# Kernel tuning notes

Hardware: AMD Instinct MI355X
Metric: run time of the kernel (lower is better)

The kernel has to match this reference:

```python
import jax, jax.numpy as jnp
import numpy as np

D_MODEL = 1024
N_HEADS = 16
D_HEAD = D_MODEL // N_HEADS
D_FF = 4 * D_MODEL
SEQ = 2048
BATCH = 4
EPS = 1e-5


def setup_inputs() -> dict:
    key = jax.random.key(0)
    ks = jax.random.split(key, 12)
    s = 0.02
    return {
        "x": jax.random.normal(ks[0], (BATCH, SEQ, D_MODEL), dtype=jnp.float32),
        "ln1_g": jnp.ones((D_MODEL,), jnp.float32),
        "ln1_b": jnp.zeros((D_MODEL,), jnp.float32),
        "wq": jax.random.normal(ks[1], (N_HEADS, D_MODEL, D_HEAD), jnp.float32) * s,
        "bq": jnp.zeros((N_HEADS, D_HEAD), jnp.float32),
        "wk": jax.random.normal(ks[2], (N_HEADS, D_MODEL, D_HEAD), jnp.float32) * s,
        "bk": jnp.zeros((N_HEADS, D_HEAD), jnp.float32),
        "wv": jax.random.normal(ks[3], (N_HEADS, D_MODEL, D_HEAD), jnp.float32) * s,
        "bv": jnp.zeros((N_HEADS, D_HEAD), jnp.float32),
        "wp": jax.random.normal(ks[4], (D_MODEL, D_MODEL), jnp.float32) * s,
        "bp": jnp.zeros((D_MODEL,), jnp.float32),
        "ln2_g": jnp.ones((D_MODEL,), jnp.float32),
        "ln2_b": jnp.zeros((D_MODEL,), jnp.float32),
        "w1": jax.random.normal(ks[5], (D_MODEL, D_FF), jnp.float32) * s,
        "b1": jnp.zeros((D_FF,), jnp.float32),
        "w2": jax.random.normal(ks[6], (D_FF, D_MODEL), jnp.float32) * s,
        "b2": jnp.zeros((D_MODEL,), jnp.float32),
    }


def _layer_norm(x, g, b):
    mu = jnp.mean(x, axis=-1, keepdims=True)
    var = jnp.mean(jnp.square(x - mu), axis=-1, keepdims=True)
    return (x - mu) * jax.lax.rsqrt(var + EPS) * g + b


def _block(x, ln1_g, ln1_b, wq, bq, wk, bk, wv, bv, wp, bp,
           ln2_g, ln2_b, w1, b1, w2, b2):
    B, S, D = x.shape
    # --- pre-LN multi-head causal self-attention ---
    xn = _layer_norm(x, ln1_g, ln1_b)
    q = jnp.einsum('bsd,hde->bhse', xn, wq) + bq[None, :, None, :]
    k = jnp.einsum('bsd,hde->bhse', xn, wk) + bk[None, :, None, :]
    v = jnp.einsum('bsd,hde->bhse', xn, wv) + bv[None, :, None, :]
    scores = jnp.einsum('bhse,bhte->bhst', q, k) / np.sqrt(D_HEAD).astype(np.float32)
    causal = jnp.tril(jnp.ones((S, S), dtype=bool))
    scores = jnp.where(causal[None, None], scores, jnp.float32(-jnp.inf))
    attn = jax.nn.softmax(scores, axis=-1)
    o = jnp.einsum('bhst,bhte->bhse', attn, v)          # [B,H,S,Dh]
    o = o.transpose(0, 2, 1, 3).reshape(B, S, D)         # concat heads
    x = x + o @ wp + bp
    # --- pre-LN feedforward ---
    xn2 = _layer_norm(x, ln2_g, ln2_b)
    h = jax.nn.relu(xn2 @ w1 + b1)
    x = x + h @ w2 + b2
    return x


def reference(x, ln1_g, ln1_b, wq, bq, wk, bk, wv, bv, wp, bp,
              ln2_g, ln2_b, w1, b1, w2, b2):
    return _block(x, ln1_g, ln1_b, wq, bq, wk, bk, wv, bv, wp, bp,
                  ln2_g, ln2_b, w1, b1, w2, b2)
```

## Files before the change

kernel.cpp:

```cpp
#include <hip/hip_runtime.h>
#include <hip/hip_bf16.h>

#define D_MODEL 1024
#define N_HEADS 16
#define D_HEAD  64
#define D_FF    4096
#define SEQ     2048
#define BATCH   4
#define NROWS   (BATCH * SEQ)

typedef __attribute__((ext_vector_type(8))) short short8;
typedef __attribute__((ext_vector_type(4))) float f32x4;

#define EXP2(x) exp2f(x)

static __device__ __forceinline__ ushort f2bf(float x) {
  __hip_bfloat16 h = __float2bfloat16(x);
  return *reinterpret_cast<ushort*>(&h);
}

static __device__ __forceinline__ void gl_lds16(const ushort* g, ushort* l) {
  __builtin_amdgcn_global_load_lds(
      (const __attribute__((address_space(1))) void*)g,
      (__attribute__((address_space(3))) void*)l, 16, 0, 0);
}

__global__ __launch_bounds__(256) void transpose_pack_b(
    const float* __restrict__ in, ushort* __restrict__ out,
    int K, int N, size_t in_bs, size_t out_bs) {
  in  += (size_t)blockIdx.z * in_bs;
  out += (size_t)blockIdx.z * out_bs;
  __shared__ float tile[32][33];
  int n0 = blockIdx.x * 32, k0 = blockIdx.y * 32;
  int tx = threadIdx.x, ty = threadIdx.y;
#pragma unroll
  for (int i = 0; i < 32; i += 8)
    tile[ty + i][tx] = in[(size_t)(k0 + ty + i) * N + n0 + tx];
  __syncthreads();
#pragma unroll
  for (int i = 0; i < 32; i += 8)
    out[(size_t)(n0 + ty + i) * K + k0 + tx] = f2bf(tile[tx][ty + i]);
}

__global__ __launch_bounds__(256) void transpose_v(
    const ushort* __restrict__ v, ushort* __restrict__ vt) {
  const int s0 = blockIdx.x * 64;
  const int bh = blockIdx.y, bb = bh >> 4, hh = bh & 15;
  __shared__ ushort tile[64][66];
  const ushort* src = v + (size_t)bb * SEQ * D_MODEL + (size_t)hh * 64;
  const int tx = threadIdx.x;
#pragma unroll
  for (int i = threadIdx.y; i < 64; i += 4)
    tile[i][tx] = src[(size_t)(s0 + i) * D_MODEL + tx];
  __syncthreads();
  ushort* dst = vt + (size_t)bh * 64 * SEQ + s0;
#pragma unroll
  for (int d = threadIdx.y; d < 64; d += 4)
    dst[(size_t)d * SEQ + tx] = tile[tx][d];
}

__global__ __launch_bounds__(256) void ln_kernel(
    const float* __restrict__ x, const float* __restrict__ g,
    const float* __restrict__ b, ushort* __restrict__ out) {
  int row = blockIdx.x, t = threadIdx.x;
  const float4 v = *(const float4*)(x + (size_t)row * D_MODEL + t * 4);
  float s  = v.x + v.y + v.z + v.w;
  float ss = v.x * v.x + v.y * v.y + v.z * v.z + v.w * v.w;
#pragma unroll
  for (int off = 1; off < 64; off <<= 1) {
    s  += __shfl_xor(s, off, 64);
    ss += __shfl_xor(ss, off, 64);
  }
  __shared__ float rs_[4], rss_[4];
  int w = t >> 6;
  if ((t & 63) == 0) { rs_[w] = s; rss_[w] = ss; }
  __syncthreads();
  s  = rs_[0] + rs_[1] + rs_[2] + rs_[3];
  ss = rss_[0] + rss_[1] + rss_[2] + rss_[3];
  float mu  = s * (1.0f / D_MODEL);
  float var = ss * (1.0f / D_MODEL) - mu * mu;
  float rstd = rsqrtf(var + 1e-5f);
  float4 gg = *(const float4*)(g + t * 4);
  float4 bb = *(const float4*)(b + t * 4);
  ushort4 r;
  r.x = f2bf((v.x - mu) * rstd * gg.x + bb.x);
  r.y = f2bf((v.y - mu) * rstd * gg.y + bb.y);
  r.z = f2bf((v.z - mu) * rstd * gg.z + bb.z);
  r.w = f2bf((v.w - mu) * rstd * gg.w + bb.w);
  *(ushort4*)(out + (size_t)row * D_MODEL + t * 4) = r;
}

template <int MODE>
__global__ __launch_bounds__(512, 2) void gemm256(
    const ushort* __restrict__ A, const ushort* __restrict__ BT,
    int M, int N, int K,
    const float* __restrict__ bias0, const float* __restrict__ bias1,
    const float* __restrict__ bias2,
    void* __restrict__ out0, void* __restrict__ out1, void* __restrict__ out2) {
  __shared__ __align__(16) ushort As[2][256 * 64];
  __shared__ __align__(16) ushort Bs[2][256 * 64];
  const int gx = N >> 8;
  const int nwg = gx * (M >> 8);
  const int cpx = nwg >> 3;
  const int tile = (blockIdx.x & 7) * cpx + (blockIdx.x >> 3);
  const int bn = tile % gx, bm = tile / gx;
  const int t = threadIdx.x, lane = t & 63, w = t >> 6;
  const int wr = w >> 2, wc = w & 3;
  const int l16 = lane & 15, l4 = lane >> 4;

  const ushort* Ab = A + (size_t)(bm * 256) * K;
  const ushort* Bb = BT + (size_t)(bn * 256) * K;

  int srow[4], scol[4];
#pragma unroll
  for (int i = 0; i < 4; ++i) {
    int c = i * 512 + t;
    srow[i] = c >> 3;
    scol[i] = 8 * ((c & 7) ^ ((c >> 3) & 7));
  }

  f32x4 acc[8][4] = {};
  int cur = 0;
  const int nk = K >> 6;

#pragma unroll
  for (int i = 0; i < 4; ++i) {
    gl_lds16(&Ab[(size_t)srow[i] * K + scol[i]], (ushort*)&As[0][(i * 512 + w * 64) * 8]);
    gl_lds16(&Bb[(size_t)srow[i] * K + scol[i]], (ushort*)&Bs[0][(i * 512 + w * 64) * 8]);
  }

  for (int kt = 0; kt < nk; ++kt) {
    if (kt + 1 < nk) {
      const int k0n = (kt + 1) << 6;
#pragma unroll
      for (int i = 0; i < 4; ++i) {
        gl_lds16(&Ab[(size_t)srow[i] * K + k0n + scol[i]], (ushort*)&As[cur ^ 1][(i * 512 + w * 64) * 8]);
        gl_lds16(&Bb[(size_t)srow[i] * K + k0n + scol[i]], (ushort*)&Bs[cur ^ 1][(i * 512 + w * 64) * 8]);
      }
      asm volatile("s_waitcnt vmcnt(8)" ::: "memory");
    } else {
      asm volatile("s_waitcnt vmcnt(0)" ::: "memory");
    }
    __builtin_amdgcn_s_barrier();

    const ushort* As_ = As[cur];
    const ushort* Bs_ = Bs[cur];
    short8 bfr[4][2];
#pragma unroll
    for (int n = 0; n < 4; ++n) {
      const int row = wc * 64 + n * 16 + l16;
      const int sw = (row & 7) * 8;
      bfr[n][0] = *(const short8*)&Bs_[row * 64 + ((l4 * 8) ^ sw)];
      bfr[n][1] = *(const short8*)&Bs_[row * 64 + ((l4 * 8 + 32) ^ sw)];
    }
#pragma unroll
    for (int m = 0; m < 8; ++m) {
      const int row = wr * 128 + m * 16 + l16;
      const int sw = (row & 7) * 8;
      short8 a0 = *(const short8*)&As_[row * 64 + ((l4 * 8) ^ sw)];
      short8 a1 = *(const short8*)&As_[row * 64 + ((l4 * 8 + 32) ^ sw)];
#pragma unroll
      for (int n = 0; n < 4; ++n) {
        acc[m][n] = __builtin_amdgcn_mfma_f32_16x16x32_bf16(a0, bfr[n][0], acc[m][n], 0, 0, 0);
        acc[m][n] = __builtin_amdgcn_mfma_f32_16x16x32_bf16(a1, bfr[n][1], acc[m][n], 0, 0, 0);
      }
    }
    asm volatile("" ::: "memory");
    __builtin_amdgcn_s_barrier();
    cur ^= 1;
  }

  const int row0 = bm * 256 + wr * 128, col0 = bn * 256 + wc * 64;
#pragma unroll
  for (int m = 0; m < 8; ++m) {
#pragma unroll
    for (int n = 0; n < 4; ++n) {
      const int col = col0 + n * 16 + l16;
      if (MODE == 0) {
        const int which = col >> 10;
        const int c = col & 1023;
        const float* bp_ = (which == 0) ? bias0 : (which == 1) ? bias1 : bias2;
        ushort* op = (which == 0) ? (ushort*)out0 : (which == 1) ? (ushort*)out1 : (ushort*)out2;
        const float scale = (which == 0) ? 0.125f * 1.44269504f : 1.0f;
#pragma unroll
        for (int i = 0; i < 4; ++i) {
          const int row = row0 + m * 16 + l4 * 4 + i;
          op[(size_t)row * D_MODEL + c] = f2bf((acc[m][n][i] + bp_[c]) * scale);
        }
      } else {
#pragma unroll
        for (int i = 0; i < 4; ++i) {
          const int row = row0 + m * 16 + l4 * 4 + i;
          const float val = fmaxf(acc[m][n][i] + bias0[col], 0.0f);
          ((ushort*)out0)[(size_t)row * D_FF + col] = f2bf(val);
        }
      }
    }
  }
}

__global__ __launch_bounds__(512, 2) void gemm256x128(
    const ushort* __restrict__ A, const ushort* __restrict__ BT,
    int M, int N, int K,
    const float* __restrict__ bias0, const float* __restrict__ resid,
    float* __restrict__ out0) {
  __shared__ __align__(16) ushort As[2][256 * 64];
  __shared__ __align__(16) ushort Bs[2][128 * 64];
  const int gx = N >> 7;
  const int nwg = gx * (M >> 8);
  const int cpx = nwg >> 3;
  const int tile = (blockIdx.x & 7) * cpx + (blockIdx.x >> 3);
  const int bn = tile % gx, bm = tile / gx;
  const int t = threadIdx.x, lane = t & 63, w = t >> 6;
  const int wr = w >> 1, wc = w & 1;
  const int l16 = lane & 15, l4 = lane >> 4;

  const ushort* Ab = A + (size_t)(bm * 256) * K;
  const ushort* Bb = BT + (size_t)(bn * 128) * K;

  int srow[4], scol[4];
#pragma unroll
  for (int i = 0; i < 4; ++i) {
    int c = i * 512 + t;
    srow[i] = c >> 3;
    scol[i] = 8 * ((c & 7) ^ ((c >> 3) & 7));
  }

  f32x4 acc[4][4] = {};
  int cur = 0;
  const int nk = K >> 6;

#pragma unroll
  for (int i = 0; i < 4; ++i)
    gl_lds16(&Ab[(size_t)srow[i] * K + scol[i]], (ushort*)&As[0][(i * 512 + w * 64) * 8]);
#pragma unroll
  for (int i = 0; i < 2; ++i)
    gl_lds16(&Bb[(size_t)srow[i] * K + scol[i]], (ushort*)&Bs[0][(i * 512 + w * 64) * 8]);

  for (int kt = 0; kt < nk; ++kt) {
    if (kt + 1 < nk) {
      const int k0n = (kt + 1) << 6;
#pragma unroll
      for (int i = 0; i < 4; ++i)
        gl_lds16(&Ab[(size_t)srow[i] * K + k0n + scol[i]], (ushort*)&As[cur ^ 1][(i * 512 + w * 64) * 8]);
#pragma unroll
      for (int i = 0; i < 2; ++i)
        gl_lds16(&Bb[(size_t)srow[i] * K + k0n + scol[i]], (ushort*)&Bs[cur ^ 1][(i * 512 + w * 64) * 8]);
      asm volatile("s_waitcnt vmcnt(6)" ::: "memory");
    } else {
      asm volatile("s_waitcnt vmcnt(0)" ::: "memory");
    }
    __builtin_amdgcn_s_barrier();

    const ushort* As_ = As[cur];
    const ushort* Bs_ = Bs[cur];
    short8 bfr[4][2];
#pragma unroll
    for (int n = 0; n < 4; ++n) {
      const int row = wc * 64 + n * 16 + l16;
      const int sw = (row & 7) * 8;
      bfr[n][0] = *(const short8*)&Bs_[row * 64 + ((l4 * 8) ^ sw)];
      bfr[n][1] = *(const short8*)&Bs_[row * 64 + ((l4 * 8 + 32) ^ sw)];
    }
#pragma unroll
    for (int m = 0; m < 4; ++m) {
      const int row = wr * 64 + m * 16 + l16;
      const int sw = (row & 7) * 8;
      short8 a0 = *(const short8*)&As_[row * 64 + ((l4 * 8) ^ sw)];
      short8 a1 = *(const short8*)&As_[row * 64 + ((l4 * 8 + 32) ^ sw)];
#pragma unroll
      for (int n = 0; n < 4; ++n) {
        acc[m][n] = __builtin_amdgcn_mfma_f32_16x16x32_bf16(a0, bfr[n][0], acc[m][n], 0, 0, 0);
        acc[m][n] = __builtin_amdgcn_mfma_f32_16x16x32_bf16(a1, bfr[n][1], acc[m][n], 0, 0, 0);
      }
    }
    asm volatile("" ::: "memory");
    __builtin_amdgcn_s_barrier();
    cur ^= 1;
  }

  const int row0 = bm * 256 + wr * 64, col0 = bn * 128 + wc * 64;
#pragma unroll
  for (int m = 0; m < 4; ++m) {
#pragma unroll
    for (int n = 0; n < 4; ++n) {
      const int col = col0 + n * 16 + l16;
#pragma unroll
      for (int i = 0; i < 4; ++i) {
        const int row = row0 + m * 16 + l4 * 4 + i;
        const size_t idx = (size_t)row * D_MODEL + col;
        out0[idx] = acc[m][n][i] + bias0[col] + resid[idx];
      }
    }
  }
}

__global__ __launch_bounds__(256) void attn4_kernel(
    const ushort* __restrict__ Q, const ushort* __restrict__ Km,
    const ushort* __restrict__ Vt, ushort* __restrict__ O) {
  const int b = blockIdx.x;
  const int bh = (b & 7) * 8 + ((b >> 3) & 7);
  const int qt = 15 - (b >> 6);
  const int bb = bh >> 4, hh = bh & 15;
  const int t = threadIdx.x, lane = t & 63, w = t >> 6;
  const int l16 = lane & 15, l4 = lane >> 4;
  const size_t base  = (size_t)bb * SEQ * D_MODEL + (size_t)hh * 64;
  const size_t vbase = (size_t)bh * 64 * SEQ;
  const int qb = qt * 128 + w * 32;

  __shared__ __align__(16) ushort Ks[2][64 * 64];
  __shared__ __align__(16) ushort Vs[2][64 * 64];
  __shared__ __align__(16) ushort Pw[4][32 * 64];
  ushort* myP = &Pw[w][0];

  short8 qf[2][2];
#pragma unroll
  for (int qj = 0; qj < 2; ++qj)
#pragma unroll
    for (int dk = 0; dk < 2; ++dk)
      qf[qj][dk] = *(const short8*)&Q[base + (size_t)(qb + qj * 16 + l16) * D_MODEL + dk * 32 + l4 * 8];

  f32x4 oacc[4][2] = {};
  float m_i[2] = {-1e30f, -1e30f}, l_i[2] = {0.0f, 0.0f};

  const int nt = qt * 2 + 2;

#define STAGE(ktile, buf) do {                                                     \
    const int kv0_ = (ktile) * 64;                                                 \
    _Pragma("unroll")                                                              \
    for (int i_ = 0; i_ < 2; ++i_) {                                               \
      const int g_ = i_ * 256 + t;                                                 \
      const int row_ = g_ >> 3;                                                    \
      const int c8_ = ((g_ & 7) ^ (row_ & 7)) * 8;                                 \
      gl_lds16(&Km[base + (size_t)(kv0_ + row_) * D_MODEL + c8_],                  \
               (ushort*)&Ks[buf][(i_ * 256 + w * 64) * 8]);                        \
      gl_lds16(&Vt[vbase + (size_t)row_ * SEQ + kv0_ + c8_],                       \
               (ushort*)&Vs[buf][(i_ * 256 + w * 64) * 8]);                        \
    }                                                                              \
  } while (0)

  STAGE(0, 0);

  int cur = 0;
  for (int kt = 0; kt < nt; ++kt) {
    const int kv0 = kt * 64;
    if (kt + 1 < nt) {
      STAGE(kt + 1, cur ^ 1);
      asm volatile("s_waitcnt vmcnt(4)" ::: "memory");
    } else {
      asm volatile("s_waitcnt vmcnt(0)" ::: "memory");
    }
    __builtin_amdgcn_s_barrier();

    const bool active = (kv0 <= qb + 31);
    if (active) {
      const ushort* Kc = Ks[cur];
      const ushort* Vc = Vs[cur];

      f32x4 sacc[2][4] = {};
#pragma unroll
      for (int n = 0; n < 4; ++n) {
        const int r = n * 16 + l16;
        const int rs = r * 8, rx = r & 7;
#pragma unroll
        for (int dk = 0; dk < 2; ++dk) {
          short8 ak = *(const short8*)&Kc[(rs + ((dk * 4 + l4) ^ rx)) * 8];
          sacc[0][n] = __builtin_amdgcn_mfma_f32_16x16x32_bf16(ak, qf[0][dk], sacc[0][n], 0, 0, 0);
          sacc[1][n] = __builtin_amdgcn_mfma_f32_16x16x32_bf16(ak, qf[1][dk], sacc[1][n], 0, 0, 0);
        }
      }

      const bool diag = (kv0 + 63 > qb);
#pragma unroll
      for (int qj = 0; qj < 2; ++qj) {
        const int qq = qb + qj * 16 + l16;
        const int ql = qj * 16 + l16;
        const int psw = (ql & 7) * 8;
        if (diag) {
#pragma unroll
          for (int n = 0; n < 4; ++n)
#pragma unroll
            for (int i = 0; i < 4; ++i) {
              const int kv = kv0 + n * 16 + l4 * 4 + i;
              if (kv > qq) sacc[qj][n][i] = -1e30f;
            }
        }
        float mx = -1e30f;
#pragma unroll
        for (int n = 0; n < 4; ++n)
#pragma unroll
          for (int i = 0; i < 4; ++i) mx = fmaxf(mx, sacc[qj][n][i]);
        mx = fmaxf(mx, __shfl_xor(mx, 16, 64));
        mx = fmaxf(mx, __shfl_xor(mx, 32, 64));

        if (__any(mx > m_i[qj] + 8.0f)) {
          const float mnew = fmaxf(m_i[qj], mx);
          const float alpha = EXP2(m_i[qj] - mnew);
          m_i[qj] = mnew;
          l_i[qj] *= alpha;
#pragma unroll
          for (int nd = 0; nd < 4; ++nd)
#pragma unroll
            for (int i = 0; i < 4; ++i) oacc[nd][qj][i] *= alpha;
        }

        float lsum = 0.0f;
#pragma unroll
        for (int n = 0; n < 4; ++n) {
          const float p0 = EXP2(sacc[qj][n][0] - m_i[qj]);
          const float p1 = EXP2(sacc[qj][n][1] - m_i[qj]);
          const float p2 = EXP2(sacc[qj][n][2] - m_i[qj]);
          const float p3 = EXP2(sacc[qj][n][3] - m_i[qj]);
          lsum += p0 + p1 + p2 + p3;
          ushort4 pk;
          pk.x = f2bf(p0); pk.y = f2bf(p1); pk.z = f2bf(p2); pk.w = f2bf(p3);
          *(ushort4*)&myP[ql * 64 + ((n * 16 + l4 * 4) ^ psw)] = pk;
        }
        lsum += __shfl_xor(lsum, 16, 64);
        lsum += __shfl_xor(lsum, 32, 64);
        l_i[qj] += lsum;
      }

#pragma unroll
      for (int kk = 0; kk < 2; ++kk) {
        short8 bp[2];
#pragma unroll
        for (int qj = 0; qj < 2; ++qj) {
          const int ql = qj * 16 + l16;
          bp[qj] = *(const short8*)&myP[ql * 64 + ((kk * 32 + l4 * 8) ^ ((ql & 7) * 8))];
        }
#pragma unroll
        for (int nd = 0; nd < 4; ++nd) {
          const int r = nd * 16 + l16;
          short8 av = *(const short8*)&Vc[(r * 8 + ((kk * 4 + l4) ^ (r & 7))) * 8];
          oacc[nd][0] = __builtin_amdgcn_mfma_f32_16x16x32_bf16(av, bp[0], oacc[nd][0], 0, 0, 0);
          oacc[nd][1] = __builtin_amdgcn_mfma_f32_16x16x32_bf16(av, bp[1], oacc[nd][1], 0, 0, 0);
        }
      }
    }

    asm volatile("" ::: "memory");
    __builtin_amdgcn_s_barrier();
    cur ^= 1;
  }
#undef STAGE

#pragma unroll
  for (int qj = 0; qj < 2; ++qj) {
    const int qq = qb + qj * 16 + l16;
    const float inv = 1.0f / l_i[qj];
#pragma unroll
    for (int nd = 0; nd < 4; ++nd) {
      ushort4 r;
      r.x = f2bf(oacc[nd][qj][0] * inv);
      r.y = f2bf(oacc[nd][qj][1] * inv);
      r.z = f2bf(oacc[nd][qj][2] * inv);
      r.w = f2bf(oacc[nd][qj][3] * inv);
      *(ushort4*)&O[base + (size_t)qq * D_MODEL + nd * 16 + l4 * 4] = r;
    }
  }
}

extern "C" void kernel_launch(void* const* d_in, const int* in_sizes, int n_in,
                              void* d_out, int out_size, void* d_ws, size_t ws_size,
                              hipStream_t stream) {
  const float* x    = (const float*)d_in[0];
  const float* ln1g = (const float*)d_in[1];
  const float* ln1b = (const float*)d_in[2];
  const float* wq   = (const float*)d_in[3];
  const float* bq   = (const float*)d_in[4];
  const float* wk   = (const float*)d_in[5];
  const float* bk   = (const float*)d_in[6];
  const float* wv   = (const float*)d_in[7];
  const float* bv   = (const float*)d_in[8];
  const float* wp   = (const float*)d_in[9];
  const float* bp   = (const float*)d_in[10];
  const float* ln2g = (const float*)d_in[11];
  const float* ln2b = (const float*)d_in[12];
  const float* w1   = (const float*)d_in[13];
  const float* b1   = (const float*)d_in[14];
  const float* w2   = (const float*)d_in[15];
  const float* b2   = (const float*)d_in[16];
  float* out = (float*)d_out;

  char* base = (char*)d_ws;
  size_t off = 0;
  auto alloc = [&](size_t bytes) -> void* {
    void* r = base + off;
    off += (bytes + 255) & ~(size_t)255;
    return r;
  };
  ushort* WqkvT = (ushort*)alloc((size_t)3 * D_MODEL * D_MODEL * 2);
  ushort* WpT   = (ushort*)alloc((size_t)D_MODEL * D_MODEL * 2);
  ushort* W1T   = (ushort*)alloc((size_t)D_FF * D_MODEL * 2);
  ushort* W2T   = (ushort*)alloc((size_t)D_MODEL * D_FF * 2);
  ushort* xn    = (ushort*)alloc((size_t)NROWS * D_MODEL * 2);
  ushort* q     = (ushort*)alloc((size_t)NROWS * D_MODEL * 2);
  ushort* k     = (ushort*)alloc((size_t)NROWS * D_MODEL * 2);
  ushort* v     = (ushort*)alloc((size_t)NROWS * D_MODEL * 2);
  ushort* o     = (ushort*)alloc((size_t)NROWS * D_MODEL * 2);
  float*  x2    = (float*) alloc((size_t)NROWS * D_MODEL * 4);
  ushort* xn2   = (ushort*)alloc((size_t)NROWS * D_MODEL * 2);
  ushort* hbuf  = (ushort*)alloc((size_t)NROWS * D_FF * 2);
  ushort* vt = xn;

  dim3 tb(32, 8);
  transpose_pack_b<<<dim3(2, 32, 16), tb, 0, stream>>>(wq, WqkvT + (size_t)0 * D_MODEL * D_MODEL,
      D_MODEL, D_HEAD, (size_t)D_MODEL * D_HEAD, (size_t)D_HEAD * D_MODEL);
  transpose_pack_b<<<dim3(2, 32, 16), tb, 0, stream>>>(wk, WqkvT + (size_t)1 * D_MODEL * D_MODEL,
      D_MODEL, D_HEAD, (size_t)D_MODEL * D_HEAD, (size_t)D_HEAD * D_MODEL);
  transpose_pack_b<<<dim3(2, 32, 16), tb, 0, stream>>>(wv, WqkvT + (size_t)2 * D_MODEL * D_MODEL,
      D_MODEL, D_HEAD, (size_t)D_MODEL * D_HEAD, (size_t)D_HEAD * D_MODEL);
  transpose_pack_b<<<dim3(32, 32, 1), tb, 0, stream>>>(wp, WpT, D_MODEL, D_MODEL, 0, 0);
  transpose_pack_b<<<dim3(128, 32, 1), tb, 0, stream>>>(w1, W1T, D_MODEL, D_FF, 0, 0);
  transpose_pack_b<<<dim3(32, 128, 1), tb, 0, stream>>>(w2, W2T, D_FF, D_MODEL, 0, 0);

  ln_kernel<<<NROWS, 256, 0, stream>>>(x, ln1g, ln1b, xn);
  gemm256<0><<<dim3((NROWS / 256) * (3 * D_MODEL / 256)), 512, 0, stream>>>(
      xn, WqkvT, NROWS, 3 * D_MODEL, D_MODEL, bq, bk, bv, q, k, v);
  transpose_v<<<dim3(SEQ / 64, BATCH * N_HEADS), dim3(64, 4), 0, stream>>>(v, vt);
  attn4_kernel<<<1024, 256, 0, stream>>>(q, k, vt, o);
  gemm256x128<<<dim3((NROWS / 256) * (D_MODEL / 128)), 512, 0, stream>>>(
      o, WpT, NROWS, D_MODEL, D_MODEL, bp, x, x2);
  ln_kernel<<<NROWS, 256, 0, stream>>>(x2, ln2g, ln2b, xn2);
  gemm256<2><<<dim3((NROWS / 256) * (D_FF / 256)), 512, 0, stream>>>(
      xn2, W1T, NROWS, D_FF, D_MODEL, b1, nullptr, nullptr, hbuf, nullptr, nullptr);
  gemm256x128<<<dim3((NROWS / 256) * (D_MODEL / 128)), 512, 0, stream>>>(
      hbuf, W2T, NROWS, D_MODEL, D_FF, b2, x2, out);
}
```

Baseline: 396.9 us.

## Restructure GEMMs into half-K panels with interleaved prefetch and MFMA priority

The two GEMM kernels now split each 64-wide K tile into two 32-wide LDS panels with a new swizzle. Global-to-LDS loads for the next tile are spread between MFMA groups, and s_setprio wraps the MFMA bursts, so memory traffic overlaps compute more finely. Fewer A/B fragments are held in registers at once. The output-projection and FFN-down GEMMs change their tile from 256x128 to 128x256, with the wave layout changed to match. The risks are a more complex waitcnt and barrier schedule and extra barriers per K step.

```diff
diff --git a/kernel.cpp b/kernel.cpp
--- a/kernel.cpp
+++ b/kernel.cpp
@@ -13,6 +13,7 @@
 typedef __attribute__((ext_vector_type(4))) float f32x4;
 
 #define EXP2(x) exp2f(x)
+#define MFMA16(a, b, c) __builtin_amdgcn_mfma_f32_16x16x32_bf16(a, b, c, 0, 0, 0)
 
 static __device__ __forceinline__ ushort f2bf(float x) {
   __hip_bfloat16 h = __float2bfloat16(x);
@@ -23,6 +24,10 @@
   __builtin_amdgcn_global_load_lds(
       (const __attribute__((address_space(1))) void*)g,
       (__attribute__((address_space(3))) void*)l, 16, 0, 0);
+}
+
+static __device__ __forceinline__ int panel_off(int r, int l4) {
+  return ((r >> 1) << 6) + (((((r & 1) << 2) + l4) ^ ((r >> 1) & 7)) << 3);
 }
 
 __global__ __launch_bounds__(256) void transpose_pack_b(
@@ -91,14 +96,14 @@
 }
 
 template <int MODE>
-__global__ __launch_bounds__(512, 2) void gemm256(
+__global__ __launch_bounds__(512, 2) void gemm8p256(
     const ushort* __restrict__ A, const ushort* __restrict__ BT,
     int M, int N, int K,
     const float* __restrict__ bias0, const float* __restrict__ bias1,
     const float* __restrict__ bias2,
     void* __restrict__ out0, void* __restrict__ out1, void* __restrict__ out2) {
-  __shared__ __align__(16) ushort As[2][256 * 64];
-  __shared__ __align__(16) ushort Bs[2][256 * 64];
+  __shared__ __align__(16) ushort AL[2][2][256 * 32];
+  __shared__ __align__(16) ushort BL[2][2][256 * 32];
   const int gx = N >> 8;
   const int nwg = gx * (M >> 8);
   const int cpx = nwg >> 3;
@@ -111,63 +116,103 @@
   const ushort* Ab = A + (size_t)(bm * 256) * K;
   const ushort* Bb = BT + (size_t)(bn * 256) * K;
 
-  int srow[4], scol[4];
-#pragma unroll
-  for (int i = 0; i < 4; ++i) {
+  int sr[2], sg[2];
+#pragma unroll
+  for (int i = 0; i < 2; ++i) {
     int c = i * 512 + t;
-    srow[i] = c >> 3;
-    scol[i] = 8 * ((c & 7) ^ ((c >> 3) & 7));
-  }
+    int p = c >> 3, slog = (c & 7) ^ (p & 7);
+    sr[i] = p * 2 + (slog >> 2);
+    sg[i] = (slog & 3) * 8;
+  }
+  int aoff[8], boff[4];
+#pragma unroll
+  for (int m = 0; m < 8; ++m) aoff[m] = panel_off(wr * 128 + m * 16 + l16, l4);
+#pragma unroll
+  for (int n = 0; n < 4; ++n) boff[n] = panel_off(wc * 64 + n * 16 + l16, l4);
 
   f32x4 acc[8][4] = {};
+  const int nk = K >> 6;
+
+  auto stageA = [&](int buf, int kk, int kc) {
+#pragma unroll
+    for (int i = 0; i < 2; ++i)
+      gl_lds16(&Ab[(size_t)sr[i] * K + kc + kk * 32 + sg[i]],
+               &AL[buf][kk][(i * 512 + w * 64) * 8]);
+  };
+  auto stageB = [&](int buf, int kk, int kc) {
+#pragma unroll
+    for (int i = 0; i < 2; ++i)
+      gl_lds16(&Bb[(size_t)sr[i] * K + kc + kk * 32 + sg[i]],
+               &BL[buf][kk][(i * 512 + w * 64) * 8]);
+  };
+
+  stageA(0, 0, 0); stageB(0, 0, 0); stageA(0, 1, 0); stageB(0, 1, 0);
+  asm volatile("s_waitcnt vmcnt(4)" ::: "memory");
+  __builtin_amdgcn_s_barrier();
+
   int cur = 0;
-  const int nk = K >> 6;
-
-#pragma unroll
-  for (int i = 0; i < 4; ++i) {
-    gl_lds16(&Ab[(size_t)srow[i] * K + scol[i]], (ushort*)&As[0][(i * 512 + w * 64) * 8]);
-    gl_lds16(&Bb[(size_t)srow[i] * K + scol[i]], (ushort*)&Bs[0][(i * 512 + w * 64) * 8]);
-  }
-
   for (int kt = 0; kt < nk; ++kt) {
-    if (kt + 1 < nk) {
-      const int k0n = (kt + 1) << 6;
-#pragma unroll
-      for (int i = 0; i < 4; ++i) {
-        gl_lds16(&Ab[(size_t)srow[i] * K + k0n + scol[i]], (ushort*)&As[cur ^ 1][(i * 512 + w * 64) * 8]);
-        gl_lds16(&Bb[(size_t)srow[i] * K + k0n + scol[i]], (ushort*)&Bs[cur ^ 1][(i * 512 + w * 64) * 8]);
-      }
-      asm volatile("s_waitcnt vmcnt(8)" ::: "memory");
-    } else {
-      asm volatile("s_waitcnt vmcnt(0)" ::: "memory");
-    }
+    const bool pf = (kt + 1 < nk);
+    const int kc = (kt + 1) << 6;
+    const int nxt = cur ^ 1;
+    const ushort* A0 = AL[cur][0]; const ushort* A1 = AL[cur][1];
+    const ushort* B0 = BL[cur][0]; const ushort* B1 = BL[cur][1];
+    short8 aR[8], bR[2];
+
+    if (pf) stageA(nxt, 0, kc);
+#pragma unroll
+    for (int m = 0; m < 8; ++m) aR[m] = *(const short8*)&A0[aoff[m]];
+    bR[0] = *(const short8*)&B0[boff[0]];
+    bR[1] = *(const short8*)&B0[boff[1]];
+    __builtin_amdgcn_s_setprio(1);
+#pragma unroll
+    for (int m = 0; m < 8; ++m) {
+      acc[m][0] = MFMA16(aR[m], bR[0], acc[m][0]);
+      acc[m][1] = MFMA16(aR[m], bR[1], acc[m][1]);
+    }
+    __builtin_amdgcn_s_setprio(0);
+    if (pf) stageB(nxt, 0, kc);
+    bR[0] = *(const short8*)&B0[boff[2]];
+    bR[1] = *(const short8*)&B0[boff[3]];
+    __builtin_amdgcn_s_setprio(1);
+#pragma unroll
+    for (int m = 0; m < 8; ++m) {
+      acc[m][2] = MFMA16(aR[m], bR[0], acc[m][2]);
+      acc[m][3] = MFMA16(aR[m], bR[1], acc[m][3]);
+    }
+    __builtin_amdgcn_s_setprio(0);
+    if (pf) asm volatile("s_waitcnt vmcnt(4)" ::: "memory");
+    else    asm volatile("s_waitcnt vmcnt(0)" ::: "memory");
+    __builtin_amdgcn_sched_barrier(0);
     __builtin_amdgcn_s_barrier();
-
-    const ushort* As_ = As[cur];
-    const ushort* Bs_ = Bs[cur];
-    short8 bfr[4][2];
-#pragma unroll
-    for (int n = 0; n < 4; ++n) {
-      const int row = wc * 64 + n * 16 + l16;
-      const int sw = (row & 7) * 8;
-      bfr[n][0] = *(const short8*)&Bs_[row * 64 + ((l4 * 8) ^ sw)];
-      bfr[n][1] = *(const short8*)&Bs_[row * 64 + ((l4 * 8 + 32) ^ sw)];
-    }
+    if (pf) stageA(nxt, 1, kc);
+#pragma unroll
+    for (int m = 0; m < 8; ++m) aR[m] = *(const short8*)&A1[aoff[m]];
+    bR[0] = *(const short8*)&B1[boff[0]];
+    bR[1] = *(const short8*)&B1[boff[1]];
+    __builtin_amdgcn_s_setprio(1);
 #pragma unroll
     for (int m = 0; m < 8; ++m) {
-      const int row = wr * 128 + m * 16 + l16;
-      const int sw = (row & 7) * 8;
-      short8 a0 = *(const short8*)&As_[row * 64 + ((l4 * 8) ^ sw)];
-      short8 a1 = *(const short8*)&As_[row * 64 + ((l4 * 8 + 32) ^ sw)];
-#pragma unroll
-      for (int n = 0; n < 4; ++n) {
-        acc[m][n] = __builtin_amdgcn_mfma_f32_16x16x32_bf16(a0, bfr[n][0], acc[m][n], 0, 0, 0);
-        acc[m][n] = __builtin_amdgcn_mfma_f32_16x16x32_bf16(a1, bfr[n][1], acc[m][n], 0, 0, 0);
-      }
-    }
-    asm volatile("" ::: "memory");
-    __builtin_amdgcn_s_barrier();
-    cur ^= 1;
+      acc[m][0] = MFMA16(aR[m], bR[0], acc[m][0]);
+      acc[m][1] = MFMA16(aR[m], bR[1], acc[m][1]);
+    }
+    __builtin_amdgcn_s_setprio(0);
+    if (pf) stageB(nxt, 1, kc);
+    bR[0] = *(const short8*)&B1[boff[2]];
+    bR[1] = *(const short8*)&B1[boff[3]];
+    __builtin_amdgcn_s_setprio(1);
+#pragma unroll
+    for (int m = 0; m < 8; ++m) {
+      acc[m][2] = MFMA16(aR[m], bR[0], acc[m][2]);
+      acc[m][3] = MFMA16(aR[m], bR[1], acc[m][3]);
+    }
+    __builtin_amdgcn_s_setprio(0);
+    if (pf) {
+      asm volatile("s_waitcnt vmcnt(4)" ::: "memory");
+      __builtin_amdgcn_sched_barrier(0);
+      __builtin_amdgcn_s_barrier();
+    }
+    cur = nxt;
   }
 
   const int row0 = bm * 256 + wr * 128, col0 = bn * 256 + wc * 64;
@@ -199,87 +244,125 @@
   }
 }
 
-__global__ __launch_bounds__(512, 2) void gemm256x128(
+__global__ __launch_bounds__(512, 2) void gemm8p128(
     const ushort* __restrict__ A, const ushort* __restrict__ BT,
     int M, int N, int K,
     const float* __restrict__ bias0, const float* __restrict__ resid,
     float* __restrict__ out0) {
-  __shared__ __align__(16) ushort As[2][256 * 64];
-  __shared__ __align__(16) ushort Bs[2][128 * 64];
-  const int gx = N >> 7;
-  const int nwg = gx * (M >> 8);
+  __shared__ __align__(16) ushort AL[2][2][128 * 32];
+  __shared__ __align__(16) ushort BL[2][2][256 * 32];
+  const int gx = N >> 8;
+  const int nwg = gx * (M >> 7);
   const int cpx = nwg >> 3;
   const int tile = (blockIdx.x & 7) * cpx + (blockIdx.x >> 3);
   const int bn = tile % gx, bm = tile / gx;
   const int t = threadIdx.x, lane = t & 63, w = t >> 6;
-  const int wr = w >> 1, wc = w & 1;
+  const int wr = w >> 2, wc = w & 3;
   const int l16 = lane & 15, l4 = lane >> 4;
 
-  const ushort* Ab = A + (size_t)(bm * 256) * K;
-  const ushort* Bb = BT + (size_t)(bn * 128) * K;
-
-  int srow[4], scol[4];
-#pragma unroll
-  for (int i = 0; i < 4; ++i) {
+  const ushort* Ab = A + (size_t)(bm * 128) * K;
+  const ushort* Bb = BT + (size_t)(bn * 256) * K;
+
+  const int pA = t >> 3, slogA = (t & 7) ^ (pA & 7);
+  const int srA = pA * 2 + (slogA >> 2);
+  const int sgA = (slogA & 3) * 8;
+  int srB[2], sgB[2];
+#pragma unroll
+  for (int i = 0; i < 2; ++i) {
     int c = i * 512 + t;
-    srow[i] = c >> 3;
-    scol[i] = 8 * ((c & 7) ^ ((c >> 3) & 7));
-  }
+    int p = c >> 3, slog = (c & 7) ^ (p & 7);
+    srB[i] = p * 2 + (slog >> 2);
+    sgB[i] = (slog & 3) * 8;
+  }
+  int aoff[4], boff[4];
+#pragma unroll
+  for (int m = 0; m < 4; ++m) aoff[m] = panel_off(wr * 64 + m * 16 + l16, l4);
+#pragma unroll
+  for (int n = 0; n < 4; ++n) boff[n] = panel_off(wc * 64 + n * 16 + l16, l4);
 
   f32x4 acc[4][4] = {};
+  const int nk = K >> 6;
+
+  auto stageA = [&](int buf, int kk, int kc) {
+    gl_lds16(&Ab[(size_t)srA * K + kc + kk * 32 + sgA], &AL[buf][kk][(w * 64) * 8]);
+  };
+  auto stageB = [&](int buf, int kk, int kc) {
+#pragma unroll
+    for (int i = 0; i < 2; ++i)
+      gl_lds16(&Bb[(size_t)srB[i] * K + kc + kk * 32 + sgB[i]],
+               &BL[buf][kk][(i * 512 + w * 64) * 8]);
+  };
+
+  stageA(0, 0, 0); stageB(0, 0, 0); stageA(0, 1, 0); stageB(0, 1, 0);
+  asm volatile("s_waitcnt vmcnt(3)" ::: "memory");
+  __builtin_amdgcn_s_barrier();
+
   int cur = 0;
-  const int nk = K >> 6;
-
-#pragma unroll
-  for (int i = 0; i < 4; ++i)
-    gl_lds16(&Ab[(size_t)srow[i] * K + scol[i]], (ushort*)&As[0][(i * 512 + w * 64) * 8]);
-#pragma unroll
-  for (int i = 0; i < 2; ++i)
-    gl_lds16(&Bb[(size_t)srow[i] * K + scol[i]], (ushort*)&Bs[0][(i * 512 + w * 64) * 8]);
-
   for (int kt = 0; kt < nk; ++kt) {
-    if (kt + 1 < nk) {
-      const int k0n = (kt + 1) << 6;
-#pragma unroll
-      for (int i = 0; i < 4; ++i)
-        gl_lds16(&Ab[(size_t)srow[i] * K + k0n + scol[i]], (ushort*)&As[cur ^ 1][(i * 512 + w * 64) * 8]);
-#pragma unroll
-      for (int i = 0; i < 2; ++i)
-        gl_lds16(&Bb[(size_t)srow[i] * K + k0n + scol[i]], (ushort*)&Bs[cur ^ 1][(i * 512 + w * 64) * 8]);
-      asm volatile("s_waitcnt vmcnt(6)" ::: "memory");
-    } else {
-      asm volatile("s_waitcnt vmcnt(0)" ::: "memory");
-    }
+    const bool pf = (kt + 1 < nk);
+    const int kc = (kt + 1) << 6;
+    const int nxt = cur ^ 1;
+    const ushort* A0 = AL[cur][0]; const ushort* A1 = AL[cur][1];
+    const ushort* B0 = BL[cur][0]; const ushort* B1 = BL[cur][1];
+    short8 aR[4], bR[2];
+
+    if (pf) stageA(nxt, 0, kc);
+#pragma unroll
+    for (int m = 0; m < 4; ++m) aR[m] = *(const short8*)&A0[aoff[m]];
+    bR[0] = *(const short8*)&B0[boff[0]];
+    bR[1] = *(const short8*)&B0[boff[1]];
+    __builtin_amdgcn_s_setprio(1);
+#pragma unroll
+    for (int m = 0; m < 4; ++m) {
+      acc[m][0] = MFMA16(aR[m], bR[0], acc[m][0]);
+      acc[m][1] = MFMA16(aR[m], bR[1], acc[m][1]);
+    }
+    __builtin_amdgcn_s_setprio(0);
+    if (pf) stageB(nxt, 0, kc);
+    bR[0] = *(const short8*)&B0[boff[2]];
+    bR[1] = *(const short8*)&B0[boff[3]];
+    __builtin_amdgcn_s_setprio(1);
+#pragma unroll
+    for (int m = 0; m < 4; ++m) {
+      acc[m][2] = MFMA16(aR[m], bR[0], acc[m][2]);
+      acc[m][3] = MFMA16(aR[m], bR[1], acc[m][3]);
+    }
+    __builtin_amdgcn_s_setprio(0);
+    if (pf) asm volatile("s_waitcnt vmcnt(3)" ::: "memory");
+    else    asm volatile("s_waitcnt vmcnt(0)" ::: "memory");
+    __builtin_amdgcn_sched_barrier(0);
     __builtin_amdgcn_s_barrier();
-
-    const ushort* As_ = As[cur];
-    const ushort* Bs_ = Bs[cur];
-    short8 bfr[4][2];
-#pragma unroll
-    for (int n = 0; n < 4; ++n) {
-      const int row = wc * 64 + n * 16 + l16;
-      const int sw = (row & 7) * 8;
-      bfr[n][0] = *(const short8*)&Bs_[row * 64 + ((l4 * 8) ^ sw)];
-      bfr[n][1] = *(const short8*)&Bs_[row * 64 + ((l4 * 8 + 32) ^ sw)];
-    }
+    if (pf) stageA(nxt, 1, kc);
+#pragma unroll
+    for (int m = 0; m < 4; ++m) aR[m] = *(const short8*)&A1[aoff[m]];
+    bR[0] = *(const short8*)&B1[boff[0]];
+    bR[1] = *(const short8*)&B1[boff[1]];
+    __builtin_amdgcn_s_setprio(1);
 #pragma unroll
     for (int m = 0; m < 4; ++m) {
-      const int row = wr * 64 + m * 16 + l16;
-      const int sw = (row & 7) * 8;
-      short8 a0 = *(const short8*)&As_[row * 64 + ((l4 * 8) ^ sw)];
-      short8 a1 = *(const short8*)&As_[row * 64 + ((l4 * 8 + 32) ^ sw)];
-#pragma unroll
-      for (int n = 0; n < 4; ++n) {
-        acc[m][n] = __builtin_amdgcn_mfma_f32_16x16x32_bf16(a0, bfr[n][0], acc[m][n], 0, 0, 0);
-        acc[m][n] = __builtin_amdgcn_mfma_f32_16x16x32_bf16(a1, bfr[n][1], acc[m][n], 0, 0, 0);
-      }
-    }
-    asm volatile("" ::: "memory");
-    __builtin_amdgcn_s_barrier();
-    cur ^= 1;
-  }
-
-  const int row0 = bm * 256 + wr * 64, col0 = bn * 128 + wc * 64;
+      acc[m][0] = MFMA16(aR[m], bR[0], acc[m][0]);
+      acc[m][1] = MFMA16(aR[m], bR[1], acc[m][1]);
+    }
+    __builtin_amdgcn_s_setprio(0);
+    if (pf) stageB(nxt, 1, kc);
+    bR[0] = *(const short8*)&B1[boff[2]];
+    bR[1] = *(const short8*)&B1[boff[3]];
+    __builtin_amdgcn_s_setprio(1);
+#pragma unroll
+    for (int m = 0; m < 4; ++m) {
+      acc[m][2] = MFMA16(aR[m], bR[0], acc[m][2]);
+      acc[m][3] = MFMA16(aR[m], bR[1], acc[m][3]);
+    }
+    __builtin_amdgcn_s_setprio(0);
+    if (pf) {
+      asm volatile("s_waitcnt vmcnt(3)" ::: "memory");
+      __builtin_amdgcn_sched_barrier(0);
+      __builtin_amdgcn_s_barrier();
+    }
+    cur = nxt;
+  }
+
+  const int row0 = bm * 128 + wr * 64, col0 = bn * 256 + wc * 64;
 #pragma unroll
   for (int m = 0; m < 4; ++m) {
 #pragma unroll
@@ -365,8 +448,8 @@
 #pragma unroll
         for (int dk = 0; dk < 2; ++dk) {
           short8 ak = *(const short8*)&Kc[(rs + ((dk * 4 + l4) ^ rx)) * 8];
-          sacc[0][n] = __builtin_amdgcn_mfma_f32_16x16x32_bf16(ak, qf[0][dk], sacc[0][n], 0, 0, 0);
-          sacc[1][n] = __builtin_amdgcn_mfma_f32_16x16x32_bf16(ak, qf[1][dk], sacc[1][n], 0, 0, 0);
+          sacc[0][n] = MFMA16(ak, qf[0][dk], sacc[0][n]);
+          sacc[1][n] = MFMA16(ak, qf[1][dk], sacc[1][n]);
         }
       }
 
@@ -433,8 +516,8 @@
         for (int nd = 0; nd < 4; ++nd) {
           const int r = nd * 16 + l16;
           short8 av = *(const short8*)&Vc[(r * 8 + ((kk * 4 + l4) ^ (r & 7))) * 8];
-          oacc[nd][0] = __builtin_amdgcn_mfma_f32_16x16x32_bf16(av, bp[0], oacc[nd][0], 0, 0, 0);
-          oacc[nd][1] = __builtin_amdgcn_mfma_f32_16x16x32_bf16(av, bp[1], oacc[nd][1], 0, 0, 0);
+          oacc[nd][0] = MFMA16(av, bp[0], oacc[nd][0]);
+          oacc[nd][1] = MFMA16(av, bp[1], oacc[nd][1]);
         }
       }
     }
@@ -516,15 +599,15 @@
   transpose_pack_b<<<dim3(32, 128, 1), tb, 0, stream>>>(w2, W2T, D_FF, D_MODEL, 0, 0);
 
   ln_kernel<<<NROWS, 256, 0, stream>>>(x, ln1g, ln1b, xn);
-  gemm256<0><<<dim3((NROWS / 256) * (3 * D_MODEL / 256)), 512, 0, stream>>>(
+  gemm8p256<0><<<dim3((NROWS / 256) * (3 * D_MODEL / 256)), 512, 0, stream>>>(
       xn, WqkvT, NROWS, 3 * D_MODEL, D_MODEL, bq, bk, bv, q, k, v);
   transpose_v<<<dim3(SEQ / 64, BATCH * N_HEADS), dim3(64, 4), 0, stream>>>(v, vt);
   attn4_kernel<<<1024, 256, 0, stream>>>(q, k, vt, o);
-  gemm256x128<<<dim3((NROWS / 256) * (D_MODEL / 128)), 512, 0, stream>>>(
+  gemm8p128<<<dim3((NROWS / 128) * (D_MODEL / 256)), 512, 0, stream>>>(
       o, WpT, NROWS, D_MODEL, D_MODEL, bp, x, x2);
   ln_kernel<<<NROWS, 256, 0, stream>>>(x2, ln2g, ln2b, xn2);
-  gemm256<2><<<dim3((NROWS / 256) * (D_FF / 256)), 512, 0, stream>>>(
+  gemm8p256<2><<<dim3((NROWS / 256) * (D_FF / 256)), 512, 0, stream>>>(
       xn2, W1T, NROWS, D_FF, D_MODEL, b1, nullptr, nullptr, hbuf, nullptr, nullptr);
-  gemm256x128<<<dim3((NROWS / 256) * (D_MODEL / 128)), 512, 0, stream>>>(
+  gemm8p128<<<dim3((NROWS / 128) * (D_MODEL / 256)), 512, 0, stream>>>(
       hbuf, W2T, NROWS, D_MODEL, D_FF, b2, x2, out);
 }
```

After: 482.1 us. 1.21x slower.
